# Optimization experiments

Hardware: AMD Instinct MI355X
Metric: run time of the kernel (lower is better)

Reference implementation:

```python
import jax, jax.numpy as jnp
import numpy as np

WIN = 8     # sliding-chunk window size (Long2DSCSelfAttention default w=8)
HEADS = 8   # num_heads


def setup_inputs() -> dict:
    key = jax.random.key(0)
    ks = jax.random.split(key, 3)
    B, C, H, W = 4, 512, 64, 64
    x = jax.random.normal(ks[0], (B, C, H, W), jnp.float32)
    w_qkv = jax.random.normal(ks[1], (3 * C, C), jnp.float32) * 0.02
    b_qkv = jnp.zeros((3 * C,), jnp.float32)
    w_proj = jax.random.normal(ks[2], (C, C), jnp.float32) * 0.02
    b_proj = jnp.zeros((C,), jnp.float32)
    return {"x": x, "w_qkv": w_qkv, "b_qkv": b_qkv, "w_proj": w_proj, "b_proj": b_proj}


def _chunk(t, nh, nw, win):
    B, _, _, h, d = t.shape
    t = t.reshape(B, nh, win, nw, win, h, d)
    return t.transpose(0, 5, 1, 3, 2, 4, 6).reshape(B, h, nh, nw, win * win, d)


def reference(x, w_qkv, b_qkv, w_proj, b_proj):
    B, C, H, W = x.shape
    win, heads = WIN, HEADS
    d = C // heads
    nh, nw = H // win, W // win
    m = win * win  # tokens per chunk

    xf = x.transpose(0, 2, 3, 1)                      # [B,H,W,C]
    qkv = xf @ w_qkv.T + b_qkv                        # [B,H,W,3C]
    qkv = qkv.reshape(B, H, W, 3, heads, d)
    q = _chunk(qkv[..., 0, :, :], nh, nw, win)        # [B,h,nh,nw,m,d]
    k = _chunk(qkv[..., 1, :, :], nh, nw, win)
    v = _chunk(qkv[..., 2, :, :], nh, nw, win)

    # pad chunk grid by one chunk on each side; gather 3x3 chunk neighborhoods
    kp = jnp.pad(k, ((0, 0), (0, 0), (1, 1), (1, 1), (0, 0), (0, 0)))
    vp = jnp.pad(v, ((0, 0), (0, 0), (1, 1), (1, 1), (0, 0), (0, 0)))
    k9 = jnp.concatenate([kp[:, :, i:i + nh, j:j + nw] for i in range(3) for j in range(3)], axis=4)  # [B,h,nh,nw,9m,d]
    v9 = jnp.concatenate([vp[:, :, i:i + nh, j:j + nw] for i in range(3) for j in range(3)], axis=4)

    # validity mask for neighbor chunks at the image boundary
    valid = jnp.pad(jnp.ones((nh, nw), bool), ((1, 1), (1, 1)))
    vmask = jnp.concatenate(
        [jnp.repeat(valid[i:i + nh, j:j + nw][..., None], m, axis=-1) for i in range(3) for j in range(3)],
        axis=-1)                                      # [nh,nw,9m]

    scale = float(d) ** -0.5
    attn = jnp.einsum('bhxyqd,bhxykd->bhxyqk', q * scale, k9)      # [B,h,nh,nw,m,9m]
    neg = jnp.asarray(-1e9, attn.dtype)
    attn = jnp.where(vmask[None, None, :, :, None, :], attn, neg)
    attn = jax.nn.softmax(attn, axis=-1)
    out = jnp.einsum('bhxyqk,bhxykd->bhxyqd', attn, v9)            # [B,h,nh,nw,m,d]

    out = out.reshape(B, heads, nh, nw, win, win, d)
    out = out.transpose(0, 2, 4, 3, 5, 1, 6).reshape(B, H, W, C)
    out = out @ w_proj.T + b_proj
    return out.transpose(0, 3, 1, 2)                               # [B,C,H,W]
```

## Files before the change

### kernel.cpp

```cpp
#include <hip/hip_runtime.h>
#include <cstdint>
#include <cstddef>

namespace {

constexpr int kC = 512;
constexpr int kHW = 4096;
constexpr int kHeads = 8;
constexpr int kChunkElems = 64 * 64;

typedef float f32x4 __attribute__((ext_vector_type(4)));
typedef __bf16 bf16x8 __attribute__((ext_vector_type(8)));
typedef _Float16 f16x8 __attribute__((ext_vector_type(8)));
union FragU { uint4 u; bf16x8 b; f16x8 h; };

__device__ __forceinline__ ushort bf16rn(float x) {
  uint u = __float_as_uint(x);
  return (ushort)((u + 0x7fffu + ((u >> 16) & 1u)) >> 16);
}
__device__ __forceinline__ ushort f16rn(float x) {
  _Float16 h = (_Float16)x;
  ushort u;
  __builtin_memcpy(&u, &h, 2);
  return u;
}
__device__ __forceinline__ void split2(float x, ushort& h, ushort& l) {
  ushort hh = bf16rn(x);
  float hf = __uint_as_float(((uint)hh) << 16);
  h = hh;
  l = bf16rn(x - hf);
}
__device__ __forceinline__ uint pack2(ushort a, ushort b) {
  return (uint)a | ((uint)b << 16);
}
__device__ __forceinline__ void gld16(const void* g, void* lds) {
  __builtin_amdgcn_global_load_lds(
      (const __attribute__((address_space(1))) uint32_t*)g,
      (__attribute__((address_space(3))) uint32_t*)lds, 16, 0, 0);
}

__global__ __launch_bounds__(256)
void convw_kernel(const float* __restrict__ w,
                  ushort* __restrict__ wh, ushort* __restrict__ wl)
{
  int idx = (blockIdx.x * 256 + threadIdx.x) * 8;
  float4 v0 = *(const float4*)(w + idx);
  float4 v1 = *(const float4*)(w + idx + 4);
  float xs[8] = {v0.x, v0.y, v0.z, v0.w, v1.x, v1.y, v1.z, v1.w};
  ushort hh[8], ll[8];
#pragma unroll
  for (int e = 0; e < 8; ++e) split2(xs[e], hh[e], ll[e]);
  *(uint4*)(wh + idx) = make_uint4(pack2(hh[0], hh[1]), pack2(hh[2], hh[3]),
                                   pack2(hh[4], hh[5]), pack2(hh[6], hh[7]));
  *(uint4*)(wl + idx) = make_uint4(pack2(ll[0], ll[1]), pack2(ll[2], ll[3]),
                                   pack2(ll[4], ll[5]), pack2(ll[6], ll[7]));
}

__global__ __launch_bounds__(256)
void convw16_kernel(const float* __restrict__ w, ushort* __restrict__ wh)
{
  int idx = (blockIdx.x * 256 + threadIdx.x) * 8;
  float4 v0 = *(const float4*)(w + idx);
  float4 v1 = *(const float4*)(w + idx + 4);
  float xs[8] = {v0.x, v0.y, v0.z, v0.w, v1.x, v1.y, v1.z, v1.w};
  ushort hh[8];
#pragma unroll
  for (int e = 0; e < 8; ++e) hh[e] = f16rn(xs[e]);
  *(uint4*)(wh + idx) = make_uint4(pack2(hh[0], hh[1]), pack2(hh[2], hh[3]),
                                   pack2(hh[4], hh[5]), pack2(hh[6], hh[7]));
}

__global__ __launch_bounds__(256)
void convx_kernel(const float* __restrict__ x, ushort* __restrict__ xt)
{
  __shared__ float LT[64][68];
  const int tid = threadIdx.x;
  const int t0 = blockIdx.x * 64;
  const int c0 = blockIdx.y * 64;
  const int b  = blockIdx.z;
  const float* xb = x + (size_t)b * kC * kHW;

#pragma unroll
  for (int u = 0; u < 4; ++u) {
    int idx = tid + u * 256;
    int rc = idx >> 4;
    int t4 = (idx & 15) << 2;
    float4 val = *(const float4*)(xb + (size_t)(c0 + rc) * kHW + t0 + t4);
    LT[t4 + 0][rc] = val.x;
    LT[t4 + 1][rc] = val.y;
    LT[t4 + 2][rc] = val.z;
    LT[t4 + 3][rc] = val.w;
  }
  __syncthreads();
#pragma unroll
  for (int u = 0; u < 4; ++u) {
    int idx = tid + u * 256;
    int rt = idx >> 4;
    int c4 = (idx & 15) << 2;
    float4 v = *(const float4*)&LT[rt][c4];
    size_t o = ((size_t)b * kHW + t0 + rt) * kC + c0 + c4;
    *(ushort4*)(xt + o) = make_ushort4(f16rn(v.x), f16rn(v.y),
                                       f16rn(v.z), f16rn(v.w));
  }
}

__global__ __launch_bounds__(256)
void qkv_mfma_kernel(const ushort* __restrict__ xt,
                     const ushort* __restrict__ wq,
                     const float* __restrict__ bqkv,
                     ushort* __restrict__ qo, ushort* __restrict__ ko,
                     ushort* __restrict__ vo)
{
  __shared__ __align__(16) ushort As[128 * 64];
  __shared__ __align__(16) ushort Bs[128 * 64];

  const int tid  = threadIdx.x;
  const int lane = tid & 63;
  const int wv   = tid >> 6;
  const int quad = lane >> 4;
  const int l15  = lane & 15;
  const int wm = wv & 1, wn = wv >> 1;
  const int m0 = blockIdx.x * 128;
  const int n0 = blockIdx.y * 128;
  const int b  = blockIdx.z;

  const ushort* xb = xt + (size_t)b * kHW * kC;

  f32x4 acc[4][4];
#pragma unroll
  for (int i = 0; i < 4; ++i)
#pragma unroll
    for (int j = 0; j < 4; ++j) acc[i][j] = (f32x4){0.f, 0.f, 0.f, 0.f};

  for (int k0 = 0; k0 < kC; k0 += 64) {
    __syncthreads();
#pragma unroll
    for (int ii = 0; ii < 4; ++ii) {
      int i = wv * 4 + ii;
      int m = i * 8 + (lane >> 3);
      int gch = (lane & 7) ^ (m & 7);
      size_t goA = (size_t)(m0 + m) * kC + k0 + gch * 8;
      gld16(xb + goA, (char*)As + i * 1024);
      size_t goB = (size_t)(n0 + m) * kC + k0 + gch * 8;
      gld16(wq + goB, (char*)Bs + i * 1024);
    }
    __syncthreads();

#pragma unroll
    for (int s = 0; s < 2; ++s) {
      const int gq = s * 4 + quad;
      FragU aA[4], bB[4];
#pragma unroll
      for (int mi = 0; mi < 4; ++mi) {
        int mr = wm * 64 + mi * 16 + l15;
        int off = mr * 64 + ((gq ^ (mr & 7)) * 8);
        aA[mi].u = *(const uint4*)&As[off];
      }
#pragma unroll
      for (int ni = 0; ni < 4; ++ni) {
        int nr = wn * 64 + ni * 16 + l15;
        int off = nr * 64 + ((gq ^ (nr & 7)) * 8);
        bB[ni].u = *(const uint4*)&Bs[off];
      }
#pragma unroll
      for (int mi = 0; mi < 4; ++mi)
#pragma unroll
        for (int ni = 0; ni < 4; ++ni)
          acc[mi][ni] = __builtin_amdgcn_mfma_f32_16x16x32_f16(aA[mi].h, bB[ni].h, acc[mi][ni], 0, 0, 0);
    }
  }

  const int sec = n0 >> 9;
  const int jwbase = n0 + wn * 64;
  const int head = (jwbase >> 6) & 7;
  const size_t hbb = ((size_t)b * kHeads + head) * 64;
  float biasv[4];
#pragma unroll
  for (int ni = 0; ni < 4; ++ni) biasv[ni] = bqkv[jwbase + ni * 16 + l15];

  if (sec == 2) {
#pragma unroll
    for (int ni = 0; ni < 4; ++ni) {
      int dd = ni * 16 + l15;
#pragma unroll
      for (int mi = 0; mi < 4; ++mi) {
        int t0t = m0 + wm * 64 + mi * 16 + quad * 4;
        int h = t0t >> 6, w = t0t & 63;
        int cy = h >> 3, iy = h & 7, cx = w >> 3, ix = w & 7;
        size_t cb = (hbb + cy * 8 + cx) * (size_t)kChunkElems;
        int tokb = iy * 8 + ix;
        ushort hh[4];
#pragma unroll
        for (int r = 0; r < 4; ++r) hh[r] = f16rn(acc[mi][ni][r] + biasv[ni]);
        *(ushort4*)(vo + cb + (size_t)dd * 64 + tokb) = make_ushort4(hh[0], hh[1], hh[2], hh[3]);
      }
    }
  } else {
    __syncthreads();
    ushort* dst = (sec == 0) ? qo : ko;
    const float sc = (sec == 0) ? 0.125f : 1.0f;
    ushort* tH = As + wv * 1152;
    const int ltok = lane >> 2;
    const int dd0 = (lane & 3) * 16;
#pragma unroll
    for (int mi = 0; mi < 4; ++mi) {
#pragma unroll
      for (int ni = 0; ni < 4; ++ni)
#pragma unroll
        for (int r = 0; r < 4; ++r)
          tH[(quad * 4 + r) * 68 + ni * 16 + l15] =
              f16rn((acc[mi][ni][r] + biasv[ni]) * sc);
      int tg = m0 + wm * 64 + mi * 16 + ltok;
      int h = tg >> 6, w = tg & 63;
      int cy = h >> 3, iy = h & 7, cx = w >> 3, ix = w & 7;
      size_t cb = (hbb + cy * 8 + cx) * (size_t)kChunkElems
                + (size_t)(iy * 8 + ix) * 64 + dd0;
      uint4 h0 = *(const uint4*)&tH[ltok * 68 + dd0];
      uint4 h1 = *(const uint4*)&tH[ltok * 68 + dd0 + 8];
      *(uint4*)(dst + cb) = h0;
      *(uint4*)(dst + cb + 8) = h1;
    }
  }
}

__global__ __launch_bounds__(256)
void attn_mfma_kernel(const ushort* __restrict__ qg, const ushort* __restrict__ kg,
                      const ushort* __restrict__ vg,
                      ushort* __restrict__ aoh, ushort* __restrict__ aol)
{
  __shared__ __align__(16) ushort KB[4096], VB[4096];
  __shared__ __align__(16) ushort Ps[4 * 16 * 72];

  const int tid  = threadIdx.x;
  const int lane = tid & 63;
  const int wv   = tid >> 6;
  const int quad = lane >> 4;
  const int l15  = lane & 15;

  const int bx = blockIdx.x;
  const int g  = (bx & 7) * 4 + ((bx >> 3) >> 6);
  const int c  = (bx >> 3) & 63;
  const int b = g >> 3, head = g & 7;
  const int cy = c >> 3, cx = c & 7;

  const size_t hb = (size_t)b * kHeads + head;
  const size_t cbase = (hb * 64 + cy * 8 + cx) * (size_t)kChunkElems;

  FragU aQ0, aQ1;
  {
    const ushort* qr = qg + cbase + (size_t)(wv * 16 + l15) * 64 + quad * 8;
    aQ0.u = *(const uint4*)(qr);
    aQ1.u = *(const uint4*)(qr + 32);
  }

  const int boff = ((lane >> 3) * 64) + (((lane & 7) ^ (lane >> 3)) * 8);

  f32x4 o[4];
  float rsum[4];
#pragma unroll
  for (int r = 0; r < 4; ++r) {
    o[r] = (f32x4){0.f, 0.f, 0.f, 0.f};
    rsum[r] = 0.f;
  }

  for (int dy = -1; dy <= 1; ++dy) {
    for (int dx = -1; dx <= 1; ++dx) {
      int ncy = cy + dy, ncx = cx + dx;
      if (ncy < 0 || ncy >= 8 || ncx < 0 || ncx >= 8) continue;
      const size_t nb = (hb * 64 + ncy * 8 + ncx) * (size_t)kChunkElems;

      __syncthreads();
#pragma unroll
      for (int ii = 0; ii < 2; ++ii) {
        int ikb = wv * 2 + ii;
        size_t go = nb + (size_t)ikb * 512 + boff;
        gld16(kg + go, (char*)KB + ikb * 1024);
        gld16(vg + go, (char*)VB + ikb * 1024);
      }
      __syncthreads();

      f32x4 s[4];
#pragma unroll
      for (int nt = 0; nt < 4; ++nt) s[nt] = (f32x4){0.f, 0.f, 0.f, 0.f};
#pragma unroll
      for (int nt = 0; nt < 4; ++nt) {
        int row = nt * 16 + l15;
        int sw = l15 & 7;
        int off0 = row * 64 + ((quad ^ sw) * 8);
        int off1 = row * 64 + (((4 + quad) ^ sw) * 8);
        FragU b0, b1;
        b0.u = *(const uint4*)&KB[off0];
        b1.u = *(const uint4*)&KB[off1];
        s[nt] = __builtin_amdgcn_mfma_f32_16x16x32_f16(aQ0.h, b0.h, s[nt], 0, 0, 0);
        s[nt] = __builtin_amdgcn_mfma_f32_16x16x32_f16(aQ1.h, b1.h, s[nt], 0, 0, 0);
      }

#pragma unroll
      for (int r = 0; r < 4; ++r) {
        int prow = wv * 16 * 72 + (quad * 4 + r) * 72;
#pragma unroll
        for (int nt = 0; nt < 4; ++nt) {
          float e = __expf(s[nt][r]);
          rsum[r] += e;
          Ps[prow + nt * 16 + l15] = f16rn(e);
        }
      }

      FragU aP0, aP1;
      aP0.u = *(const uint4*)&Ps[wv * 16 * 72 + l15 * 72 + quad * 8];
      aP1.u = *(const uint4*)&Ps[wv * 16 * 72 + l15 * 72 + 32 + quad * 8];
#pragma unroll
      for (int nt = 0; nt < 4; ++nt) {
        int row = nt * 16 + l15;
        int sw = l15 & 7;
        int off0 = row * 64 + ((quad ^ sw) * 8);
        int off1 = row * 64 + (((4 + quad) ^ sw) * 8);
        FragU v0, v1;
        v0.u = *(const uint4*)&VB[off0];
        v1.u = *(const uint4*)&VB[off1];
        o[nt] = __builtin_amdgcn_mfma_f32_16x16x32_f16(aP0.h, v0.h, o[nt], 0, 0, 0);
        o[nt] = __builtin_amdgcn_mfma_f32_16x16x32_f16(aP1.h, v1.h, o[nt], 0, 0, 0);
      }
    }
  }

  float inv[4];
#pragma unroll
  for (int r = 0; r < 4; ++r) {
    float t = rsum[r];
#pragma unroll
    for (int m = 1; m < 16; m <<= 1) t += __shfl_xor(t, m, 64);
    inv[r] = 1.0f / t;
  }

  ushort* Pw = Ps + wv * 16 * 72;
  const int ltok = lane >> 2;
  const int c0 = (lane & 3) * 16;
  int trg = wv * 16 + ltok;
  int hp = cy * 8 + (trg >> 3);
  int wp = cx * 8 + (trg & 7);
  size_t obase = ((size_t)b * kHW + hp * 64 + wp) * (size_t)kC + head * 64 + c0;

#pragma unroll
  for (int r = 0; r < 4; ++r)
#pragma unroll
    for (int nt = 0; nt < 4; ++nt)
      Pw[(quad * 4 + r) * 72 + nt * 16 + l15] = bf16rn(o[nt][r] * inv[r]);
  {
    uint4 u0 = *(const uint4*)&Pw[ltok * 72 + c0];
    uint4 u1 = *(const uint4*)&Pw[ltok * 72 + c0 + 8];
    *(uint4*)(aoh + obase) = u0;
    *(uint4*)(aoh + obase + 8) = u1;
  }
#pragma unroll
  for (int r = 0; r < 4; ++r)
#pragma unroll
    for (int nt = 0; nt < 4; ++nt) {
      float val = o[nt][r] * inv[r];
      ushort hh, ll;
      split2(val, hh, ll);
      Pw[(quad * 4 + r) * 72 + nt * 16 + l15] = ll;
    }
  {
    uint4 u0 = *(const uint4*)&Pw[ltok * 72 + c0];
    uint4 u1 = *(const uint4*)&Pw[ltok * 72 + c0 + 8];
    *(uint4*)(aol + obase) = u0;
    *(uint4*)(aol + obase + 8) = u1;
  }
}

__global__ __launch_bounds__(256)
void proj_mfma_kernel(const ushort* __restrict__ aoh, const ushort* __restrict__ aol,
                      const ushort* __restrict__ wph, const ushort* __restrict__ wpl,
                      const float* __restrict__ bproj,
                      float* __restrict__ out)
{
  __shared__ __align__(16) ushort AsH[128 * 64], AsL[128 * 64];
  __shared__ __align__(16) ushort BsH[64 * 64],  BsL[64 * 64];

  const int tid  = threadIdx.x;
  const int lane = tid & 63;
  const int wv   = tid >> 6;
  const int quad = lane >> 4;
  const int l15  = lane & 15;
  const int wm = wv & 1, wn = wv >> 1;
  const int n0g = blockIdx.x * 64;
  const int m0  = blockIdx.y * 128;
  const int b   = n0g >> 12;
  const int tl0 = n0g & 4095;

  f32x4 acc[4][2];
#pragma unroll
  for (int i = 0; i < 4; ++i)
#pragma unroll
    for (int j = 0; j < 2; ++j) acc[i][j] = (f32x4){0.f, 0.f, 0.f, 0.f};

  for (int k0 = 0; k0 < kC; k0 += 64) {
    __syncthreads();
#pragma unroll
    for (int ii = 0; ii < 4; ++ii) {
      int i = wv * 4 + ii;
      int m = i * 8 + (lane >> 3);
      int gch = (lane & 7) ^ (m & 7);
      size_t goA = (size_t)(m0 + m) * kC + k0 + gch * 8;
      gld16(wph + goA, (char*)AsH + i * 1024);
      gld16(wpl + goA, (char*)AsL + i * 1024);
    }
#pragma unroll
    for (int ii = 0; ii < 2; ++ii) {
      int i = wv * 2 + ii;
      int m = i * 8 + (lane >> 3);
      int gch = (lane & 7) ^ (m & 7);
      size_t goB = (size_t)(n0g + m) * kC + k0 + gch * 8;
      gld16(aoh + goB, (char*)BsH + i * 1024);
      gld16(aol + goB, (char*)BsL + i * 1024);
    }
    __syncthreads();

#pragma unroll
    for (int s = 0; s < 2; ++s) {
      const int gq = s * 4 + quad;
      FragU aH[4], aL[4], bH[2], bL[2];
#pragma unroll
      for (int mi = 0; mi < 4; ++mi) {
        int mr = wm * 64 + mi * 16 + l15;
        int off = mr * 64 + ((gq ^ (mr & 7)) * 8);
        aH[mi].u = *(const uint4*)&AsH[off];
        aL[mi].u = *(const uint4*)&AsL[off];
      }
#pragma unroll
      for (int ni = 0; ni < 2; ++ni) {
        int nr = wn * 32 + ni * 16 + l15;
        int off = nr * 64 + ((gq ^ (nr & 7)) * 8);
        bH[ni].u = *(const uint4*)&BsH[off];
        bL[ni].u = *(const uint4*)&BsL[off];
      }
#pragma unroll
      for (int mi = 0; mi < 4; ++mi)
#pragma unroll
        for (int ni = 0; ni < 2; ++ni) {
          acc[mi][ni] = __builtin_amdgcn_mfma_f32_16x16x32_bf16(aH[mi].b, bH[ni].b, acc[mi][ni], 0, 0, 0);
          acc[mi][ni] = __builtin_amdgcn_mfma_f32_16x16x32_bf16(aH[mi].b, bL[ni].b, acc[mi][ni], 0, 0, 0);
          acc[mi][ni] = __builtin_amdgcn_mfma_f32_16x16x32_bf16(aL[mi].b, bH[ni].b, acc[mi][ni], 0, 0, 0);
        }
    }
  }

#pragma unroll
  for (int mi = 0; mi < 4; ++mi)
#pragma unroll
    for (int r = 0; r < 4; ++r) {
      int c = m0 + wm * 64 + mi * 16 + quad * 4 + r;
      float bias = bproj[c];
      size_t rowb = ((size_t)b * kC + c) * (size_t)kHW + tl0 + wn * 32;
#pragma unroll
      for (int ni = 0; ni < 2; ++ni)
        out[rowb + ni * 16 + l15] = acc[mi][ni][r] + bias;
    }
}

}

extern "C" void kernel_launch(void* const* d_in, const int* in_sizes, int n_in,
                              void* d_out, int out_size, void* d_ws, size_t ws_size,
                              hipStream_t stream)
{
  const float* x     = (const float*)d_in[0];
  const float* wqkv  = (const float*)d_in[1];
  const float* bqkv  = (const float*)d_in[2];
  const float* wproj = (const float*)d_in[3];
  const float* bproj = (const float*)d_in[4];
  float* out = (float*)d_out;

  const size_t seg = (size_t)2048 * kChunkElems;
  ushort* base = (ushort*)d_ws;
  ushort* qb = base + 0 * seg;
  ushort* kb = base + 1 * seg;
  ushort* vb = base + 2 * seg;
  ushort* xt = base + 3 * seg;
  ushort* ao_hi = xt;
  ushort* ao_lo = base + 4 * seg;
  ushort* wqh = base + 5 * seg;
  ushort* wph = qb;
  ushort* wpl = qb + 262144;

  convw16_kernel<<<dim3(384), 256, 0, stream>>>(wqkv, wqh);
  convx_kernel<<<dim3(64, 8, 4), 256, 0, stream>>>(x, xt);
  qkv_mfma_kernel<<<dim3(32, 12, 4), 256, 0, stream>>>(xt, wqh, bqkv,
                                                       qb, kb, vb);
  attn_mfma_kernel<<<dim3(2048), 256, 0, stream>>>(qb, kb, vb, ao_hi, ao_lo);
  convw_kernel<<<dim3(128), 256, 0, stream>>>(wproj, wph, wpl);
  proj_mfma_kernel<<<dim3(256, 4), 256, 0, stream>>>(ao_hi, ao_lo, wph, wpl, bproj, out);
}
```

Measured before the change: 203.8 us.

## Double-buffer K/V neighbor chunks and transpose MFMA operands in attention kernel

The attention kernel now keeps two K/V buffers in shared memory and prefetches the next valid neighbor chunk while computing on the current one. It relies on manual vmcnt waits and barriers instead of two __syncthreads per neighbor. The MFMA operands are swapped so each lane holds a full token row of scores. This makes the row-sum reduction a two-step shuffle and lets P and the output be written as packed ushort4 stores straight to global memory, skipping the LDS transpose. The cost is twice the LDS for K/V, which may lower occupancy, and the hand-written waitcnt sequence is fragile.

```diff
diff --git a/kernel.cpp b/kernel.cpp
--- a/kernel.cpp
+++ b/kernel.cpp
@@ -228,7 +228,7 @@
                       const ushort* __restrict__ vg,
                       ushort* __restrict__ aoh, ushort* __restrict__ aol)
 {
-  __shared__ __align__(16) ushort KB[4096], VB[4096];
+  __shared__ __align__(16) ushort KB[2][4096], VB[2][4096];
   __shared__ __align__(16) ushort Ps[4 * 16 * 72];
 
   const int tid  = threadIdx.x;
@@ -254,118 +254,123 @@
   }
 
   const int boff = ((lane >> 3) * 64) + (((lane & 7) ^ (lane >> 3)) * 8);
+  ushort* PsW = Ps + wv * 1152;
+
+  auto stage = [&](int buf, size_t nb) {
+#pragma unroll
+    for (int ii = 0; ii < 2; ++ii) {
+      int ikb = wv * 2 + ii;
+      size_t go = nb + (size_t)ikb * 512 + boff;
+      gld16(kg + go, (char*)&KB[buf][0] + ikb * 1024);
+      gld16(vg + go, (char*)&VB[buf][0] + ikb * 1024);
+    }
+  };
+  auto nvalid = [&](int t) -> bool {
+    int ny = cy + t / 3 - 1, nx = cx + t % 3 - 1;
+    return (unsigned)ny < 8u && (unsigned)nx < 8u;
+  };
+  auto nbase = [&](int t) -> size_t {
+    int ny = cy + t / 3 - 1, nx = cx + t % 3 - 1;
+    return (hb * 64 + ny * 8 + nx) * (size_t)kChunkElems;
+  };
 
   f32x4 o[4];
-  float rsum[4];
-#pragma unroll
-  for (int r = 0; r < 4; ++r) {
-    o[r] = (f32x4){0.f, 0.f, 0.f, 0.f};
-    rsum[r] = 0.f;
-  }
-
-  for (int dy = -1; dy <= 1; ++dy) {
-    for (int dx = -1; dx <= 1; ++dx) {
-      int ncy = cy + dy, ncx = cx + dx;
-      if (ncy < 0 || ncy >= 8 || ncx < 0 || ncx >= 8) continue;
-      const size_t nb = (hb * 64 + ncy * 8 + ncx) * (size_t)kChunkElems;
-
-      __syncthreads();
-#pragma unroll
-      for (int ii = 0; ii < 2; ++ii) {
-        int ikb = wv * 2 + ii;
-        size_t go = nb + (size_t)ikb * 512 + boff;
-        gld16(kg + go, (char*)KB + ikb * 1024);
-        gld16(vg + go, (char*)VB + ikb * 1024);
-      }
-      __syncthreads();
-
-      f32x4 s[4];
-#pragma unroll
-      for (int nt = 0; nt < 4; ++nt) s[nt] = (f32x4){0.f, 0.f, 0.f, 0.f};
-#pragma unroll
-      for (int nt = 0; nt < 4; ++nt) {
-        int row = nt * 16 + l15;
-        int sw = l15 & 7;
-        int off0 = row * 64 + ((quad ^ sw) * 8);
-        int off1 = row * 64 + (((4 + quad) ^ sw) * 8);
-        FragU b0, b1;
-        b0.u = *(const uint4*)&KB[off0];
-        b1.u = *(const uint4*)&KB[off1];
-        s[nt] = __builtin_amdgcn_mfma_f32_16x16x32_f16(aQ0.h, b0.h, s[nt], 0, 0, 0);
-        s[nt] = __builtin_amdgcn_mfma_f32_16x16x32_f16(aQ1.h, b1.h, s[nt], 0, 0, 0);
-      }
-
-#pragma unroll
-      for (int r = 0; r < 4; ++r) {
-        int prow = wv * 16 * 72 + (quad * 4 + r) * 72;
-#pragma unroll
-        for (int nt = 0; nt < 4; ++nt) {
-          float e = __expf(s[nt][r]);
-          rsum[r] += e;
-          Ps[prow + nt * 16 + l15] = f16rn(e);
-        }
-      }
-
-      FragU aP0, aP1;
-      aP0.u = *(const uint4*)&Ps[wv * 16 * 72 + l15 * 72 + quad * 8];
-      aP1.u = *(const uint4*)&Ps[wv * 16 * 72 + l15 * 72 + 32 + quad * 8];
-#pragma unroll
-      for (int nt = 0; nt < 4; ++nt) {
-        int row = nt * 16 + l15;
-        int sw = l15 & 7;
-        int off0 = row * 64 + ((quad ^ sw) * 8);
-        int off1 = row * 64 + (((4 + quad) ^ sw) * 8);
-        FragU v0, v1;
-        v0.u = *(const uint4*)&VB[off0];
-        v1.u = *(const uint4*)&VB[off1];
-        o[nt] = __builtin_amdgcn_mfma_f32_16x16x32_f16(aP0.h, v0.h, o[nt], 0, 0, 0);
-        o[nt] = __builtin_amdgcn_mfma_f32_16x16x32_f16(aP1.h, v1.h, o[nt], 0, 0, 0);
-      }
-    }
-  }
-
-  float inv[4];
-#pragma unroll
-  for (int r = 0; r < 4; ++r) {
-    float t = rsum[r];
-#pragma unroll
-    for (int m = 1; m < 16; m <<= 1) t += __shfl_xor(t, m, 64);
-    inv[r] = 1.0f / t;
-  }
-
-  ushort* Pw = Ps + wv * 16 * 72;
-  const int ltok = lane >> 2;
-  const int c0 = (lane & 3) * 16;
-  int trg = wv * 16 + ltok;
-  int hp = cy * 8 + (trg >> 3);
-  int wp = cx * 8 + (trg & 7);
-  size_t obase = ((size_t)b * kHW + hp * 64 + wp) * (size_t)kC + head * 64 + c0;
-
-#pragma unroll
-  for (int r = 0; r < 4; ++r)
-#pragma unroll
-    for (int nt = 0; nt < 4; ++nt)
-      Pw[(quad * 4 + r) * 72 + nt * 16 + l15] = bf16rn(o[nt][r] * inv[r]);
-  {
-    uint4 u0 = *(const uint4*)&Pw[ltok * 72 + c0];
-    uint4 u1 = *(const uint4*)&Pw[ltok * 72 + c0 + 8];
-    *(uint4*)(aoh + obase) = u0;
-    *(uint4*)(aoh + obase + 8) = u1;
-  }
-#pragma unroll
-  for (int r = 0; r < 4; ++r)
+#pragma unroll
+  for (int r = 0; r < 4; ++r) o[r] = (f32x4){0.f, 0.f, 0.f, 0.f};
+  float rsum = 0.f;
+
+  int t = 0;
+  while (!nvalid(t)) ++t;
+  stage(0, nbase(t));
+  int cur = 0;
+
+  for (;;) {
+    int tn = t + 1;
+    while (tn < 9 && !nvalid(tn)) ++tn;
+    const bool more = (tn < 9);
+    if (more) {
+      stage(cur ^ 1, nbase(tn));
+      asm volatile("s_waitcnt vmcnt(4)" ::: "memory");
+    } else {
+      asm volatile("s_waitcnt vmcnt(0)" ::: "memory");
+    }
+    asm volatile("s_barrier" ::: "memory");
+
+    const ushort* KBc = &KB[cur][0];
+    const ushort* VBc = &VB[cur][0];
+
+    f32x4 s[4];
+#pragma unroll
+    for (int nt = 0; nt < 4; ++nt) s[nt] = (f32x4){0.f, 0.f, 0.f, 0.f};
 #pragma unroll
     for (int nt = 0; nt < 4; ++nt) {
-      float val = o[nt][r] * inv[r];
-      ushort hh, ll;
-      split2(val, hh, ll);
-      Pw[(quad * 4 + r) * 72 + nt * 16 + l15] = ll;
-    }
-  {
-    uint4 u0 = *(const uint4*)&Pw[ltok * 72 + c0];
-    uint4 u1 = *(const uint4*)&Pw[ltok * 72 + c0 + 8];
-    *(uint4*)(aol + obase) = u0;
-    *(uint4*)(aol + obase + 8) = u1;
+      int row = nt * 16 + l15;
+      int sw = l15 & 7;
+      int off0 = row * 64 + ((quad ^ sw) * 8);
+      int off1 = row * 64 + (((4 + quad) ^ sw) * 8);
+      FragU k0, k1;
+      k0.u = *(const uint4*)&KBc[off0];
+      k1.u = *(const uint4*)&KBc[off1];
+      s[nt] = __builtin_amdgcn_mfma_f32_16x16x32_f16(k0.h, aQ0.h, s[nt], 0, 0, 0);
+      s[nt] = __builtin_amdgcn_mfma_f32_16x16x32_f16(k1.h, aQ1.h, s[nt], 0, 0, 0);
+    }
+
+#pragma unroll
+    for (int nt = 0; nt < 4; ++nt) {
+      float e0 = __expf(s[nt][0]);
+      float e1 = __expf(s[nt][1]);
+      float e2 = __expf(s[nt][2]);
+      float e3 = __expf(s[nt][3]);
+      rsum += (e0 + e1) + (e2 + e3);
+      *(ushort4*)&PsW[l15 * 72 + nt * 16 + quad * 4] =
+          make_ushort4(f16rn(e0), f16rn(e1), f16rn(e2), f16rn(e3));
+    }
+
+    FragU aP0, aP1;
+    aP0.u = *(const uint4*)&PsW[l15 * 72 + quad * 8];
+    aP1.u = *(const uint4*)&PsW[l15 * 72 + 32 + quad * 8];
+
+#pragma unroll
+    for (int nt = 0; nt < 4; ++nt) {
+      int row = nt * 16 + l15;
+      int sw = l15 & 7;
+      int off0 = row * 64 + ((quad ^ sw) * 8);
+      int off1 = row * 64 + (((4 + quad) ^ sw) * 8);
+      FragU v0, v1;
+      v0.u = *(const uint4*)&VBc[off0];
+      v1.u = *(const uint4*)&VBc[off1];
+      o[nt] = __builtin_amdgcn_mfma_f32_16x16x32_f16(v0.h, aP0.h, o[nt], 0, 0, 0);
+      o[nt] = __builtin_amdgcn_mfma_f32_16x16x32_f16(v1.h, aP1.h, o[nt], 0, 0, 0);
+    }
+
+    if (!more) break;
+    asm volatile("s_barrier" ::: "memory");
+    cur ^= 1;
+    t = tn;
+  }
+
+  rsum += __shfl_xor(rsum, 16, 64);
+  rsum += __shfl_xor(rsum, 32, 64);
+  const float inv = 1.0f / rsum;
+
+  const int trg = wv * 16 + l15;
+  const int hp = cy * 8 + (trg >> 3);
+  const int wp = cx * 8 + (trg & 7);
+  const size_t obase = ((size_t)b * kHW + hp * 64 + wp) * (size_t)kC + head * 64;
+
+#pragma unroll
+  for (int nt = 0; nt < 4; ++nt) {
+    float v0 = o[nt][0] * inv;
+    float v1 = o[nt][1] * inv;
+    float v2 = o[nt][2] * inv;
+    float v3 = o[nt][3] * inv;
+    *(ushort4*)(aoh + obase + nt * 16 + quad * 4) =
+        make_ushort4(bf16rn(v0), bf16rn(v1), bf16rn(v2), bf16rn(v3));
+    ushort h0, l0, h1, l1, h2, l2, h3, l3;
+    split2(v0, h0, l0); split2(v1, h1, l1);
+    split2(v2, h2, l2); split2(v3, h3, l3);
+    *(ushort4*)(aol + obase + nt * 16 + quad * 4) =
+        make_ushort4(l0, l1, l2, l3);
   }
 }
 
```

Result: faster. 196.1 us (-3.8%).
